# Kernel tuning notes

Hardware: AMD Instinct MI355X
Metric: run time of the kernel (lower is better)

Reference implementation:

```python
import jax, jax.numpy as jnp
import numpy as np

B, S, E, H = 2, 2048, 1024, 16
D = E // H
SCALE = D ** -0.5


def setup_inputs() -> dict:
    key = jax.random.key(0)
    k1, k2, k3, k4, k5 = jax.random.split(key, 5)
    x = jax.random.normal(k1, (B, S, E), dtype=jnp.float32)
    # torch Linear weights: [out, in]
    W_attn = jax.random.normal(k2, (3 * E, E), dtype=jnp.float32) * (E ** -0.5)
    b_attn = jax.random.normal(k3, (3 * E,), dtype=jnp.float32) * 0.02
    W_proj = jax.random.normal(k4, (E, E), dtype=jnp.float32) * (E ** -0.5)
    b_proj = jax.random.normal(k5, (E,), dtype=jnp.float32) * 0.02
    mask = jnp.tril(jnp.ones((S, S), dtype=jnp.int32))[None, None]  # causal [1,1,S,S]
    return {"x": x, "W_attn": W_attn, "b_attn": b_attn,
            "W_proj": W_proj, "b_proj": b_proj, "mask": mask}


def reference(x, W_attn, b_attn, W_proj, b_proj, mask):
    # fused qkv projection: [B,S,3E]
    qkv = jnp.einsum('bse,fe->bsf', x, W_attn) + b_attn
    q, k, v = jnp.split(qkv, 3, axis=-1)
    # split heads -> [B,H,S,D]
    def heads(t):
        return t.reshape(B, S, H, D).transpose(0, 2, 1, 3)
    q, k, v = heads(q), heads(k), heads(v)
    # scaled dot-product attention with causal mask
    w = jnp.einsum('bhqd,bhkd->bhqk', q, k) * SCALE
    w = jnp.where(mask == 0, jnp.finfo(w.dtype).min, w)
    w = jax.nn.softmax(w, axis=-1)  # attn dropout p=0 (eval)
    o = jnp.einsum('bhqk,bhkd->bhqd', w, v)
    # merge heads -> [B,S,E]
    o = o.transpose(0, 2, 1, 3).reshape(B, S, E)
    out = jnp.einsum('bse,fe->bsf', o, W_proj) + b_proj  # resid dropout p=0
    return out
```

## Files before the change

### kernel.cpp

```cpp
#include <hip/hip_runtime.h>
#include <hip/hip_bf16.h>

typedef unsigned short u16;
typedef unsigned int u32;
typedef float f32x4 __attribute__((ext_vector_type(4)));
typedef short bf16x8 __attribute__((ext_vector_type(8)));

#define BB 2
#define SS 2048
#define EE 1024
#define HH 16
#define DD 64
#define QSCALE 0.18033688011f

__device__ __forceinline__ u16 f2bf(float f) {
    union { u32 i; float f; } x; x.f = f;
    return (u16)((x.i + 0x7FFFu + ((x.i >> 16) & 1u)) >> 16);
}
__device__ __forceinline__ u32 pkbf(float a, float b) {
    __hip_bfloat162 h = __float22bfloat162_rn(make_float2(a, b));
    union { __hip_bfloat162 h; u32 u; } c; c.h = h; return c.u;
}

#define MFMA16(a, b, c) __builtin_amdgcn_mfma_f32_16x16x32_bf16((a), (b), (c), 0, 0, 0)

__device__ __forceinline__ void gld16(const u16* g, u16* l) {
    __builtin_amdgcn_global_load_lds(
        (const __attribute__((address_space(1))) void*)g,
        (__attribute__((address_space(3))) void*)l,
        16, 0, 0);
}

__global__ __launch_bounds__(256) void convert_all(
    const float* __restrict__ x, const float* __restrict__ wa,
    const float* __restrict__ wp, u16* __restrict__ dst)
{
    const size_t n0 = (size_t)4096 * 1024;
    const size_t n1 = n0 + (size_t)3072 * 1024;
    size_t i = ((size_t)blockIdx.x * 256 + threadIdx.x) * 4;
    const float* s;
    size_t off;
    if (i < n0)      { s = x;  off = 0;  }
    else if (i < n1) { s = wa; off = n0; }
    else             { s = wp; off = n1; }
    float4 v = *(const float4*)(s + (i - off));
    uint2 o;
    o.x = pkbf(v.x, v.y);
    o.y = pkbf(v.z, v.w);
    *(uint2*)(dst + i) = o;
}

__global__ __launch_bounds__(512, 4) void gemm_qkv(
    const u16* __restrict__ A, const u16* __restrict__ B, const float* __restrict__ bias,
    u16* __restrict__ Qo, u16* __restrict__ Ko, u16* __restrict__ Vto)
{
    __shared__ __align__(16) u16 SMEM[2][16384];
    const int n0 = blockIdx.x * 128, m0 = blockIdx.y * 128;
    const int tid = threadIdx.x;
    const int wave = tid >> 6, lane = tid & 63;
    const int l16 = lane & 15, quad = lane >> 4;
    const int wm = wave >> 2, wn = wave & 3;
    const int ldr = lane >> 3;
    const int csw = ((lane & 7) ^ ldr) * 8;

    f32x4 acc[4][2];
#pragma unroll
    for (int i = 0; i < 4; ++i)
#pragma unroll
        for (int j = 0; j < 2; ++j) acc[i][j] = f32x4{0.f, 0.f, 0.f, 0.f};

    const int aorb = wave >> 2;
    const u16* stgsrc = aorb ? B : A;
    const int stgbase = aorb ? n0 : m0;
    const int stgoff = aorb ? 8192 : 0;

    auto stage = [&](int k0, int buf) {
        u16* stgbuf = &SMEM[buf][stgoff];
#pragma unroll
        for (int t = 0; t < 4; ++t) {
            const int c = (wave & 3) * 4 + t;
            const int row = c * 8 + ldr;
            gld16(stgsrc + (size_t)(stgbase + row) * 1024 + k0 + csw,
                  &stgbuf[c * 512 + lane * 8]);
        }
    };

    stage(0, 0);
    for (int k0 = 0; k0 < 1024; k0 += 64) {
        const int cur = (k0 >> 6) & 1;
        __syncthreads();
        if (k0 + 64 < 1024) stage(k0 + 64, cur ^ 1);
        const u16* As = SMEM[cur];
        const u16* Bs = SMEM[cur] + 8192;
#pragma unroll
        for (int ks = 0; ks < 2; ++ks) {
            bf16x8 af[4], bf[2];
#pragma unroll
            for (int i = 0; i < 4; ++i)
                af[i] = *(const bf16x8*)&As[(wm * 64 + i * 16 + l16) * 64 +
                                            ((ks * 4 + quad) ^ (l16 & 7)) * 8];
#pragma unroll
            for (int j = 0; j < 2; ++j)
                bf[j] = *(const bf16x8*)&Bs[(wn * 32 + j * 16 + l16) * 64 +
                                            ((ks * 4 + quad) ^ (l16 & 7)) * 8];
#pragma unroll
            for (int i = 0; i < 4; ++i)
#pragma unroll
                for (int j = 0; j < 2; ++j)
                    acc[i][j] = MFMA16(af[i], bf[j], acc[i][j]);
        }
    }

    const int part = blockIdx.x >> 3;
    const int hbase = (blockIdx.x & 7) << 1;
    if (part != 2) {
        const int h = hbase + (wn >> 1);
#pragma unroll
        for (int j = 0; j < 2; ++j) {
            const int f = n0 + wn * 32 + j * 16 + l16;
            const int d = f & 63;
            const float bj = bias[f];
#pragma unroll
            for (int i = 0; i < 4; ++i) {
#pragma unroll
                for (int r = 0; r < 4; ++r) {
                    const int m = m0 + wm * 64 + i * 16 + quad * 4 + r;
                    const int b = m >> 11, s = m & 2047;
                    const float val = acc[i][j][r] + bj;
                    if (part == 0)
                        Qo[(((size_t)(b * HH + h)) * SS + s) * DD + d] = f2bf(val * QSCALE);
                    else
                        Ko[(((size_t)(b * HH + h)) * SS + s) * DD + d] = f2bf(val);
                }
            }
        }
    } else {
        u16* T = SMEM[0];
#pragma unroll
        for (int wmr = 0; wmr < 2; ++wmr) {
            __syncthreads();
            if (wm == wmr) {
#pragma unroll
                for (int j = 0; j < 2; ++j) {
                    const float bj = bias[n0 + wn * 32 + j * 16 + l16];
#pragma unroll
                    for (int i = 0; i < 4; ++i) {
                        uint2 pw;
                        pw.x = pkbf(acc[i][j][0] + bj, acc[i][j][1] + bj);
                        pw.y = pkbf(acc[i][j][2] + bj, acc[i][j][3] + bj);
                        *(uint2*)&T[(wn * 32 + j * 16 + l16) * 72 + i * 16 + quad * 4] = pw;
                    }
                }
            }
            __syncthreads();
            const int frow = tid >> 2;
            const int qtr = tid & 3;
            const int h = hbase + (frow >> 6);
            const int d = frow & 63;
            const int mg = m0 + wmr * 64;
            const int b = mg >> 11, sbase = mg & 2047;
            u16* dstrow = Vto + (((size_t)(b * HH + h)) * DD + d) * SS + sbase;
#pragma unroll
            for (int l = 0; l < 4; ++l) {
                const int mo = qtr * 16 + l * 4;
                *(uint2*)(dstrow + mo) = *(const uint2*)&T[frow * 72 + mo];
            }
        }
    }
}

__global__ __launch_bounds__(512, 4) void gemm_proj(
    const u16* __restrict__ A, const u16* __restrict__ B, const float* __restrict__ bias,
    float* __restrict__ out)
{
    __shared__ __align__(16) u16 SMEM[2][12288];
    const int n0 = blockIdx.x * 128, m0 = blockIdx.y * 64;
    const int tid = threadIdx.x;
    const int wave = tid >> 6, lane = tid & 63;
    const int l16 = lane & 15, quad = lane >> 4;
    const int wm = wave >> 2, wn = wave & 3;
    const int ldr = lane >> 3;
    const int csw = ((lane & 7) ^ ldr) * 8;

    f32x4 acc[2][2];
#pragma unroll
    for (int i = 0; i < 2; ++i)
#pragma unroll
        for (int j = 0; j < 2; ++j) acc[i][j] = f32x4{0.f, 0.f, 0.f, 0.f};

    auto stage = [&](int k0, int buf) {
#pragma unroll
        for (int t = 0; t < 3; ++t) {
            const int c = wave * 3 + t;
            if (c < 8) {
                const int row = c * 8 + ldr;
                gld16(A + (size_t)(m0 + row) * 1024 + k0 + csw,
                      &SMEM[buf][c * 512 + lane * 8]);
            } else {
                const int c2 = c - 8;
                const int row = c2 * 8 + ldr;
                gld16(B + (size_t)(n0 + row) * 1024 + k0 + csw,
                      &SMEM[buf][4096 + c2 * 512 + lane * 8]);
            }
        }
    };

    stage(0, 0);
    for (int k0 = 0; k0 < 1024; k0 += 64) {
        const int cur = (k0 >> 6) & 1;
        __syncthreads();
        if (k0 + 64 < 1024) stage(k0 + 64, cur ^ 1);
        const u16* As = SMEM[cur];
        const u16* Bs = SMEM[cur] + 4096;
#pragma unroll
        for (int ks = 0; ks < 2; ++ks) {
            bf16x8 af[2], bf[2];
#pragma unroll
            for (int i = 0; i < 2; ++i)
                af[i] = *(const bf16x8*)&As[(wm * 32 + i * 16 + l16) * 64 +
                                            ((ks * 4 + quad) ^ (l16 & 7)) * 8];
#pragma unroll
            for (int j = 0; j < 2; ++j)
                bf[j] = *(const bf16x8*)&Bs[(wn * 32 + j * 16 + l16) * 64 +
                                            ((ks * 4 + quad) ^ (l16 & 7)) * 8];
#pragma unroll
            for (int i = 0; i < 2; ++i)
#pragma unroll
                for (int j = 0; j < 2; ++j)
                    acc[i][j] = MFMA16(af[i], bf[j], acc[i][j]);
        }
    }
#pragma unroll
    for (int j = 0; j < 2; ++j) {
        const int f = n0 + wn * 32 + j * 16 + l16;
        const float bj = bias[f];
#pragma unroll
        for (int i = 0; i < 2; ++i) {
#pragma unroll
            for (int r = 0; r < 4; ++r) {
                const int m = m0 + wm * 32 + i * 16 + quad * 4 + r;
                out[(size_t)m * EE + f] = acc[i][j][r] + bj;
            }
        }
    }
}

__global__ __launch_bounds__(512, 2) void attn(
    const u16* __restrict__ Q, const u16* __restrict__ K, const u16* __restrict__ VT,
    u16* __restrict__ O)
{
    const int y = blockIdx.y;
    const int bh = blockIdx.x;
    const int tid = threadIdx.x;
    const int wave = tid >> 6, lane = tid & 63;
    const int wq = wave >> 2;
    const int wv = wave & 3;
    const int l16 = lane & 15, quad = lane >> 4;
    const int ldr = lane >> 3;
    const int csw = ((lane & 7) ^ ldr) * 8;
    __shared__ __align__(16) u16 Ks[2][64 * 64];
    __shared__ __align__(16) u16 Vts[2][64 * 64];
    __shared__ __align__(16) u16 Ps[128 * 72];

    const u16* qptr = Q + (size_t)bh * SS * DD;
    const u16* kptr = K + (size_t)bh * SS * DD;
    const u16* vtptr = VT + (size_t)bh * DD * SS;
    const int b = bh >> 4, h = bh & 15;

    auto stage = [&](int t, int buf) {
        const int row = wave * 8 + ldr;
        gld16(kptr + (size_t)(t * 64 + row) * DD + csw,
              &Ks[buf][wave * 512 + lane * 8]);
        gld16(vtptr + (size_t)row * SS + t * 64 + csw,
              &Vts[buf][wave * 512 + lane * 8]);
    };

    for (int half = 0; half < 2; ++half) {
        const int t = half ? y : 15 - y;
        const int qt = 2 * t + wq;
        const int qrow = qt * 64 + wv * 16 + l16;
        bf16x8 bq[2];
#pragma unroll
        for (int ks = 0; ks < 2; ++ks)
            bq[ks] = *(const bf16x8*)(qptr + (size_t)qrow * DD + ks * 32 + quad * 8);

        float lp = 0.f;
        f32x4 o_acc[4];
#pragma unroll
        for (int j = 0; j < 4; ++j) o_acc[j] = f32x4{0.f, 0.f, 0.f, 0.f};

        const int kend = 2 * t + 1;

        __syncthreads();
        stage(0, 0);

        for (int kb = 0; kb <= kend; ++kb) {
            const int cur = kb & 1;
            __syncthreads();
            if (kb < kend) stage(kb + 1, cur ^ 1);

            if (kb <= qt) {
                f32x4 s[4];
#pragma unroll
                for (int j = 0; j < 4; ++j) s[j] = f32x4{0.f, 0.f, 0.f, 0.f};
                __builtin_amdgcn_s_setprio(1);
#pragma unroll
                for (int ks = 0; ks < 2; ++ks) {
#pragma unroll
                    for (int j = 0; j < 4; ++j) {
                        bf16x8 ak = *(const bf16x8*)&Ks[cur][(j * 16 + l16) * 64 +
                                                        ((ks * 4 + quad) ^ (l16 & 7)) * 8];
                        s[j] = MFMA16(ak, bq[ks], s[j]);
                    }
                }
                __builtin_amdgcn_s_setprio(0);
                if (kb == qt) {
#pragma unroll
                    for (int j = 0; j < 4; ++j)
#pragma unroll
                        for (int r = 0; r < 4; ++r) {
                            const int key = kb * 64 + j * 16 + quad * 4 + r;
                            if (key > qrow) s[j][r] = -INFINITY;
                        }
                }
#pragma unroll
                for (int j = 0; j < 4; ++j) {
                    const float p0 = __builtin_amdgcn_exp2f(s[j][0]);
                    const float p1 = __builtin_amdgcn_exp2f(s[j][1]);
                    const float p2 = __builtin_amdgcn_exp2f(s[j][2]);
                    const float p3 = __builtin_amdgcn_exp2f(s[j][3]);
                    lp += (p0 + p1) + (p2 + p3);
                    uint2 pw; pw.x = pkbf(p0, p1); pw.y = pkbf(p2, p3);
                    *(uint2*)&Ps[(wave * 16 + l16) * 72 + j * 16 + quad * 4] = pw;
                }
                __builtin_amdgcn_s_setprio(1);
#pragma unroll
                for (int ks = 0; ks < 2; ++ks) {
                    bf16x8 bp = *(const bf16x8*)&Ps[(wave * 16 + l16) * 72 +
                                                    ks * 32 + quad * 8];
#pragma unroll
                    for (int j = 0; j < 4; ++j) {
                        bf16x8 av = *(const bf16x8*)&Vts[cur][(j * 16 + l16) * 64 +
                                                        ((ks * 4 + quad) ^ (l16 & 7)) * 8];
                        o_acc[j] = MFMA16(av, bp, o_acc[j]);
                    }
                }
                __builtin_amdgcn_s_setprio(0);
            }
        }

        float l = lp;
        l += __shfl_xor(l, 16);
        l += __shfl_xor(l, 32);
        const float inv = 1.0f / l;
#pragma unroll
        for (int j = 0; j < 4; ++j) {
            uint2 o4;
            o4.x = pkbf(o_acc[j][0] * inv, o_acc[j][1] * inv);
            o4.y = pkbf(o_acc[j][2] * inv, o_acc[j][3] * inv);
            *(uint2*)&O[((size_t)(b * SS + qrow)) * EE + h * DD + j * 16 + quad * 4] = o4;
        }
    }
}

extern "C" void kernel_launch(void* const* d_in, const int* in_sizes, int n_in,
                              void* d_out, int out_size, void* d_ws, size_t ws_size,
                              hipStream_t stream) {
    const float* x      = (const float*)d_in[0];
    const float* W_attn = (const float*)d_in[1];
    const float* b_attn = (const float*)d_in[2];
    const float* W_proj = (const float*)d_in[3];
    const float* b_proj = (const float*)d_in[4];
    float* out = (float*)d_out;

    u16* xb  = (u16*)d_ws;
    u16* wab = xb + (size_t)4096 * 1024;
    u16* wpb = wab + (size_t)3072 * 1024;
    u16* qw  = wpb + (size_t)1024 * 1024;
    u16* kw  = qw + (size_t)BB * HH * SS * DD;
    u16* vtw = kw + (size_t)BB * HH * SS * DD;
    u16* ow  = xb;

    convert_all<<<8192, 256, 0, stream>>>(x, W_attn, W_proj, xb);
    gemm_qkv<<<dim3(24, 32), 512, 0, stream>>>(xb, wab, b_attn, qw, kw, vtw);
    attn<<<dim3(32, 8), 512, 0, stream>>>(qw, kw, vtw, ow);
    gemm_proj<<<dim3(8, 64), 512, 0, stream>>>(ow, wpb, b_proj, out);
}
```

Measured before the change: 190.1 us.

## Restructure causal attention to 128-row query tiles with four waves

The attention kernel drops the two-half balanced pairing of 64-row query tiles across 8 waves. Each block now owns one 128-row query tile with 4 waves, and each wave handles two 16-row query sub-blocks, so every K/V fragment read from LDS is reused by two MFMAs. The grid doubles to 16 y-blocks, launched largest-first. The projection GEMM grid swaps axes so adjacent blocks share the same weight column tile. The cost is fewer waves per block, more registers per wave, and masked work on the two diagonal key blocks per tile.

```diff
diff --git a/kernel.cpp b/kernel.cpp
--- a/kernel.cpp
+++ b/kernel.cpp
@@ -174,7 +174,7 @@
     float* __restrict__ out)
 {
     __shared__ __align__(16) u16 SMEM[2][12288];
-    const int n0 = blockIdx.x * 128, m0 = blockIdx.y * 64;
+    const int n0 = blockIdx.y * 128, m0 = blockIdx.x * 64;
     const int tid = threadIdx.x;
     const int wave = tid >> 6, lane = tid & 63;
     const int l16 = lane & 15, quad = lane >> 4;
@@ -245,16 +245,14 @@
     }
 }
 
-__global__ __launch_bounds__(512, 2) void attn(
+__global__ __launch_bounds__(256, 2) void attn(
     const u16* __restrict__ Q, const u16* __restrict__ K, const u16* __restrict__ VT,
     u16* __restrict__ O)
 {
-    const int y = blockIdx.y;
+    const int qi = 15 - (int)blockIdx.y;
     const int bh = blockIdx.x;
     const int tid = threadIdx.x;
     const int wave = tid >> 6, lane = tid & 63;
-    const int wq = wave >> 2;
-    const int wv = wave & 3;
     const int l16 = lane & 15, quad = lane >> 4;
     const int ldr = lane >> 3;
     const int csw = ((lane & 7) ^ ldr) * 8;
@@ -268,96 +266,115 @@
     const int b = bh >> 4, h = bh & 15;
 
     auto stage = [&](int t, int buf) {
-        const int row = wave * 8 + ldr;
-        gld16(kptr + (size_t)(t * 64 + row) * DD + csw,
-              &Ks[buf][wave * 512 + lane * 8]);
-        gld16(vtptr + (size_t)row * SS + t * 64 + csw,
-              &Vts[buf][wave * 512 + lane * 8]);
+#pragma unroll
+        for (int c = 0; c < 2; ++c) {
+            const int a0 = wave * 2 + c;
+            const int row = a0 * 8 + ldr;
+            gld16(kptr + (size_t)(t * 64 + row) * DD + csw,
+                  &Ks[buf][a0 * 512 + lane * 8]);
+            gld16(vtptr + (size_t)row * SS + t * 64 + csw,
+                  &Vts[buf][a0 * 512 + lane * 8]);
+        }
     };
 
-    for (int half = 0; half < 2; ++half) {
-        const int t = half ? y : 15 - y;
-        const int qt = 2 * t + wq;
-        const int qrow = qt * 64 + wv * 16 + l16;
-        bf16x8 bq[2];
+    bf16x8 bq[2][2];
+#pragma unroll
+    for (int qb = 0; qb < 2; ++qb) {
+        const int qrow = qi * 128 + wave * 32 + qb * 16 + l16;
 #pragma unroll
         for (int ks = 0; ks < 2; ++ks)
-            bq[ks] = *(const bf16x8*)(qptr + (size_t)qrow * DD + ks * 32 + quad * 8);
-
-        float lp = 0.f;
-        f32x4 o_acc[4];
-#pragma unroll
-        for (int j = 0; j < 4; ++j) o_acc[j] = f32x4{0.f, 0.f, 0.f, 0.f};
-
-        const int kend = 2 * t + 1;
-
+            bq[qb][ks] = *(const bf16x8*)(qptr + (size_t)qrow * DD + ks * 32 + quad * 8);
+    }
+
+    float lp[2] = {0.f, 0.f};
+    f32x4 o_acc[4][2];
+#pragma unroll
+    for (int j = 0; j < 4; ++j)
+#pragma unroll
+        for (int qb = 0; qb < 2; ++qb) o_acc[j][qb] = f32x4{0.f, 0.f, 0.f, 0.f};
+
+    const int kend = 2 * qi + 1;
+    stage(0, 0);
+
+    for (int kb = 0; kb <= kend; ++kb) {
+        const int cur = kb & 1;
         __syncthreads();
-        stage(0, 0);
-
-        for (int kb = 0; kb <= kend; ++kb) {
-            const int cur = kb & 1;
-            __syncthreads();
-            if (kb < kend) stage(kb + 1, cur ^ 1);
-
-            if (kb <= qt) {
-                f32x4 s[4];
-#pragma unroll
-                for (int j = 0; j < 4; ++j) s[j] = f32x4{0.f, 0.f, 0.f, 0.f};
-                __builtin_amdgcn_s_setprio(1);
-#pragma unroll
-                for (int ks = 0; ks < 2; ++ks) {
-#pragma unroll
-                    for (int j = 0; j < 4; ++j) {
-                        bf16x8 ak = *(const bf16x8*)&Ks[cur][(j * 16 + l16) * 64 +
-                                                        ((ks * 4 + quad) ^ (l16 & 7)) * 8];
-                        s[j] = MFMA16(ak, bq[ks], s[j]);
+        if (kb < kend) stage(kb + 1, cur ^ 1);
+
+        f32x4 s[4][2];
+#pragma unroll
+        for (int j = 0; j < 4; ++j)
+#pragma unroll
+            for (int qb = 0; qb < 2; ++qb) s[j][qb] = f32x4{0.f, 0.f, 0.f, 0.f};
+        __builtin_amdgcn_s_setprio(1);
+#pragma unroll
+        for (int ks = 0; ks < 2; ++ks) {
+#pragma unroll
+            for (int j = 0; j < 4; ++j) {
+                bf16x8 ak = *(const bf16x8*)&Ks[cur][(j * 16 + l16) * 64 +
+                                                ((ks * 4 + quad) ^ (l16 & 7)) * 8];
+                s[j][0] = MFMA16(ak, bq[0][ks], s[j][0]);
+                s[j][1] = MFMA16(ak, bq[1][ks], s[j][1]);
+            }
+        }
+        __builtin_amdgcn_s_setprio(0);
+
+        if (kb >= 2 * qi) {
+#pragma unroll
+            for (int qb = 0; qb < 2; ++qb) {
+                const int qrow = qi * 128 + wave * 32 + qb * 16 + l16;
+#pragma unroll
+                for (int j = 0; j < 4; ++j)
+#pragma unroll
+                    for (int r = 0; r < 4; ++r) {
+                        const int key = kb * 64 + j * 16 + quad * 4 + r;
+                        if (key > qrow) s[j][qb][r] = -INFINITY;
                     }
-                }
-                __builtin_amdgcn_s_setprio(0);
-                if (kb == qt) {
-#pragma unroll
-                    for (int j = 0; j < 4; ++j)
-#pragma unroll
-                        for (int r = 0; r < 4; ++r) {
-                            const int key = kb * 64 + j * 16 + quad * 4 + r;
-                            if (key > qrow) s[j][r] = -INFINITY;
-                        }
-                }
-#pragma unroll
-                for (int j = 0; j < 4; ++j) {
-                    const float p0 = __builtin_amdgcn_exp2f(s[j][0]);
-                    const float p1 = __builtin_amdgcn_exp2f(s[j][1]);
-                    const float p2 = __builtin_amdgcn_exp2f(s[j][2]);
-                    const float p3 = __builtin_amdgcn_exp2f(s[j][3]);
-                    lp += (p0 + p1) + (p2 + p3);
-                    uint2 pw; pw.x = pkbf(p0, p1); pw.y = pkbf(p2, p3);
-                    *(uint2*)&Ps[(wave * 16 + l16) * 72 + j * 16 + quad * 4] = pw;
-                }
-                __builtin_amdgcn_s_setprio(1);
-#pragma unroll
-                for (int ks = 0; ks < 2; ++ks) {
-                    bf16x8 bp = *(const bf16x8*)&Ps[(wave * 16 + l16) * 72 +
-                                                    ks * 32 + quad * 8];
-#pragma unroll
-                    for (int j = 0; j < 4; ++j) {
-                        bf16x8 av = *(const bf16x8*)&Vts[cur][(j * 16 + l16) * 64 +
-                                                        ((ks * 4 + quad) ^ (l16 & 7)) * 8];
-                        o_acc[j] = MFMA16(av, bp, o_acc[j]);
-                    }
-                }
-                __builtin_amdgcn_s_setprio(0);
-            }
-        }
-
-        float l = lp;
+            }
+        }
+
+#pragma unroll
+        for (int qb = 0; qb < 2; ++qb) {
+#pragma unroll
+            for (int j = 0; j < 4; ++j) {
+                const float p0 = __builtin_amdgcn_exp2f(s[j][qb][0]);
+                const float p1 = __builtin_amdgcn_exp2f(s[j][qb][1]);
+                const float p2 = __builtin_amdgcn_exp2f(s[j][qb][2]);
+                const float p3 = __builtin_amdgcn_exp2f(s[j][qb][3]);
+                lp[qb] += (p0 + p1) + (p2 + p3);
+                uint2 pw; pw.x = pkbf(p0, p1); pw.y = pkbf(p2, p3);
+                *(uint2*)&Ps[(wave * 32 + qb * 16 + l16) * 72 + j * 16 + quad * 4] = pw;
+            }
+        }
+
+        __builtin_amdgcn_s_setprio(1);
+#pragma unroll
+        for (int ks = 0; ks < 2; ++ks) {
+            bf16x8 bp0 = *(const bf16x8*)&Ps[(wave * 32 + l16) * 72 + ks * 32 + quad * 8];
+            bf16x8 bp1 = *(const bf16x8*)&Ps[(wave * 32 + 16 + l16) * 72 + ks * 32 + quad * 8];
+#pragma unroll
+            for (int j = 0; j < 4; ++j) {
+                bf16x8 av = *(const bf16x8*)&Vts[cur][(j * 16 + l16) * 64 +
+                                                ((ks * 4 + quad) ^ (l16 & 7)) * 8];
+                o_acc[j][0] = MFMA16(av, bp0, o_acc[j][0]);
+                o_acc[j][1] = MFMA16(av, bp1, o_acc[j][1]);
+            }
+        }
+        __builtin_amdgcn_s_setprio(0);
+    }
+
+#pragma unroll
+    for (int qb = 0; qb < 2; ++qb) {
+        float l = lp[qb];
         l += __shfl_xor(l, 16);
         l += __shfl_xor(l, 32);
         const float inv = 1.0f / l;
+        const int qrow = qi * 128 + wave * 32 + qb * 16 + l16;
 #pragma unroll
         for (int j = 0; j < 4; ++j) {
             uint2 o4;
-            o4.x = pkbf(o_acc[j][0] * inv, o_acc[j][1] * inv);
-            o4.y = pkbf(o_acc[j][2] * inv, o_acc[j][3] * inv);
+            o4.x = pkbf(o_acc[j][qb][0] * inv, o_acc[j][qb][1] * inv);
+            o4.y = pkbf(o_acc[j][qb][2] * inv, o_acc[j][qb][3] * inv);
             *(uint2*)&O[((size_t)(b * SS + qrow)) * EE + h * DD + j * 16 + quad * 4] = o4;
         }
     }
@@ -383,6 +400,6 @@
 
     convert_all<<<8192, 256, 0, stream>>>(x, W_attn, W_proj, xb);
     gemm_qkv<<<dim3(24, 32), 512, 0, stream>>>(xb, wab, b_attn, qw, kw, vtw);
-    attn<<<dim3(32, 8), 512, 0, stream>>>(qw, kw, vtw, ow);
-    gemm_proj<<<dim3(8, 64), 512, 0, stream>>>(ow, wpb, b_proj, out);
-}
+    attn<<<dim3(32, 16), 256, 0, stream>>>(qw, kw, vtw, ow);
+    gemm_proj<<<dim3(64, 8), 512, 0, stream>>>(ow, wpb, b_proj, out);
+}
```

Result: faster. 183.0 us (-3.7%).
